# Kernel tuning notes

Hardware: AMD Instinct MI355X
Metric: run time of the kernel (lower is better)

Reference implementation:

```python
import jax, jax.numpy as jnp
import numpy as np

# ---- config (matches init_kwargs) ----
B, C_IN, L, T = 32, 12, 1024, 64
C1, C2, K = 64, 128, 7
PAD = K // 2
NUM_CLASSES = 4
GAIN = 2.0
TH1, TH2 = 0.5, 0.5
TAU1, TAU2 = 1.0, 0.9
RESET = 0.0


def setup_inputs() -> dict:
    key = jax.random.key(0)
    ks = jax.random.split(key, 7)
    x = jax.random.normal(ks[0], (B, C_IN, L, T), dtype=jnp.float32)
    w1 = jax.random.normal(ks[1], (C1, C_IN, K), dtype=jnp.float32) * 0.1
    b1 = jax.random.normal(ks[2], (C1,), dtype=jnp.float32) * 0.01
    w2 = jax.random.normal(ks[3], (C2, C1, K), dtype=jnp.float32) * 0.05
    b2 = jax.random.normal(ks[4], (C2,), dtype=jnp.float32) * 0.01
    fc_w = jax.random.normal(ks[5], (NUM_CLASSES, C2), dtype=jnp.float32) * 0.1
    fc_b = jax.random.normal(ks[6], (NUM_CLASSES,), dtype=jnp.float32) * 0.01
    return {"x": x, "w1": w1, "b1": b1, "w2": w2, "b2": b2, "fc_w": fc_w, "fc_b": fc_b}


def _conv1d(x, w, b):
    # x: [B, Cin, L], w: [Cout, Cin, K] -> [B, Cout, L] (same padding)
    y = jax.lax.conv_general_dilated(
        x, w, window_strides=(1,), padding=[(PAD, PAD)],
        dimension_numbers=("NCW", "OIW", "NCW"))
    return y + b[None, :, None]


def _lif(v, inp, tau, thresh):
    # v <- v + (inp - v)/tau; spike = (v >= thresh); reset spiked neurons
    v = v + (inp - v) / tau
    spike = (v >= thresh).astype(inp.dtype)
    v = jnp.where(spike > 0, jnp.asarray(RESET, inp.dtype), v)
    return v, spike


def reference(x, w1, b1, w2, b2, fc_w, fc_b):
    # QuantStub/DeQuantStub are identity in the fp32 eager model.
    xs = jnp.transpose(x, (3, 0, 1, 2))  # [T, B, C_IN, L]

    def step(carry, xt):
        v1, v2, acc = carry
        h1 = _conv1d(xt, w1, b1) * GAIN
        v1, s1 = _lif(v1, h1, TAU1, TH1)
        h2 = _conv1d(s1, w2, b2) * GAIN
        v2, s2 = _lif(v2, h2, TAU2, TH2)
        return (v1, v2, acc + s2), None

    v1_0 = jnp.zeros((B, C1, L), x.dtype)
    v2_0 = jnp.zeros((B, C2, L), x.dtype)
    acc0 = jnp.zeros((B, C2, L), x.dtype)
    (_, _, acc), _ = jax.lax.scan(step, (v1_0, v2_0, acc0), xs)

    out = acc / jnp.asarray(T, x.dtype)          # [B, C2, L]
    out = jnp.mean(out, axis=-1)                  # AdaptiveAvgPool1d(1) + squeeze
    return out @ fc_w.T + fc_b                    # [B, NUM_CLASSES]
```

## Files before the change

### kernel.cpp

```cpp
#include <hip/hip_runtime.h>
#include <hip/hip_bf16.h>
#include <cstdint>

#define B_   32
#define CIN  12
#define L_   1024
#define T_   64
#define C1_  64
#define C2_  128
#define K_   7
#define PAD_ 3

typedef __attribute__((ext_vector_type(8))) short short8;
typedef __attribute__((ext_vector_type(4))) float float4v;

#define WS_S1T   0ull
#define WS_W2HI  268435456ull
#define WS_W1F   (WS_W2HI + 114688ull)
#define WS_ACCL  (WS_W1F + 32768ull)

static __device__ __forceinline__ ushort bf16_hi(float f) {
    __hip_bfloat16 h = __float2bfloat16(f);
    ushort u; __builtin_memcpy(&u, &h, 2); return u;
}
static __device__ __forceinline__ float bf16_back(ushort u) {
    __hip_bfloat16 h; __builtin_memcpy(&h, &u, 2); return __bfloat162float(h);
}

__global__ __launch_bounds__(256) void k0_prep_w2(const float* __restrict__ w2,
                                                  ushort* __restrict__ w2hi) {
    int i = blockIdx.x * 256 + threadIdx.x;
    if (i >= C2_ * K_ * C1_) return;
    int c2 = i / (K_ * C1_);
    int r_ = i % (K_ * C1_);
    int kk = r_ / C1_;
    int c1 = r_ % C1_;
    float w = w2[(c2 * C1_ + c1) * K_ + kk];
    ushort uh = bf16_hi(w);
    int h    = c1 >> 5;
    int c1r  = c1 & 31;
    int e    = c1r >> 4;
    int kq   = (c1r >> 2) & 3;
    int rr   = c1r & 3;
    int j    = e * 4 + rr;
    int mt   = c2 >> 4;
    int lane = kq * 16 + (c2 & 15);
    int o    = ((((kk * 2 + h) * 8 + mt) * 64) + lane) * 8 + j;
    w2hi[o] = uh;
}

__global__ __launch_bounds__(256) void k0_prep_w1(const float* __restrict__ w1,
                                                  ushort* __restrict__ w1f) {
    int i = blockIdx.x * 256 + threadIdx.x;
    if (i >= 16384) return;
    int j    = i & 7;
    int lane = (i >> 3) & 63;
    int mf   = (i >> 9) & 3;
    int ks   = (i >> 11) & 3;
    int cp   = i >> 13;
    int k    = ks * 32 + (lane >> 4) * 8 + j;
    int dl   = k >> 4;
    int slot = k & 15;
    int c1   = mf * 16 + (lane & 15);
    float v  = (slot < CIN && dl < K_) ? w1[(c1 * CIN + slot) * K_ + dl] : 0.0f;
    ushort hi = bf16_hi(v);
    float  rem = v - bf16_back(hi);
    ushort lo = bf16_hi(rem);
    w1f[i] = cp ? lo : hi;
}

__global__ __launch_bounds__(256, 2) void k1_conv1_mfma(const float* __restrict__ x,
                                                        const ushort* __restrict__ w1f,
                                                        const float* __restrict__ b1,
                                                        ushort* __restrict__ s1t) {
    __shared__ __align__(16) ushort S[10 * 2048];
    int tid  = threadIdx.x;
    int lane = tid & 63;
    int wl   = tid >> 6;
    int b    = blockIdx.y;
    int bx   = blockIdx.x;
    int swz  = ((bx & 7) << 5) | (bx >> 3);
    int lb   = swz * 4;

    #pragma unroll
    for (int it = 0; it < 5; ++it) {
        int u  = it * 256 + tid;
        int t  = u & 63;
        int h2 = (u >> 6) & 1;
        int lp = u >> 7;
        int gl = lb + lp - PAD_;
        bool ok = (gl >= 0) && (gl < L_);
        short8 hv, lv;
        #pragma unroll
        for (int jj = 0; jj < 8; ++jj) {
            int cin = h2 * 8 + jj;
            float v = (ok && cin < CIN)
                ? x[(((size_t)b * CIN + cin) * L_ + gl) * T_ + t] : 0.0f;
            ushort hb = bf16_hi(v);
            ushort lo = bf16_hi(v - bf16_back(hb));
            hv[jj] = (short)hb;
            lv[jj] = (short)lo;
        }
        int nt = t >> 4, t15 = t & 15;
        int base = lp * 2048 + nt * 256 + h2 * 128 + t15 * 8;
        *(short8*)&S[base]        = hv;
        *(short8*)&S[base + 1024] = lv;
    }
    __syncthreads();

    int t15 = lane & 15;
    int h2l = (lane >> 4) & 1;
    int kqh = lane >> 5;

    float4v acc[4][4];
    #pragma unroll
    for (int i = 0; i < 4; ++i)
        #pragma unroll
        for (int jn = 0; jn < 4; ++jn)
            acc[i][jn] = (float4v){0.0f, 0.0f, 0.0f, 0.0f};

    #pragma unroll
    for (int ks = 0; ks < 4; ++ks) {
        int dtap = ks * 2 + kqh;
        int lpr  = (dtap == 7) ? 0 : (wl + dtap);
        int rb   = lpr * 2048 + h2l * 128 + t15 * 8;
        short8 bh[4], bl[4];
        #pragma unroll
        for (int nt = 0; nt < 4; ++nt) {
            bh[nt] = *(const short8*)&S[rb + nt * 256];
            bl[nt] = *(const short8*)&S[rb + nt * 256 + 1024];
        }
        #pragma unroll
        for (int mf = 0; mf < 4; ++mf) {
            const ushort* ap = w1f + ((size_t)(ks * 4 + mf) * 64 + lane) * 8;
            short8 ah = *(const short8*)ap;
            short8 al = *(const short8*)(ap + 8192);
            #pragma unroll
            for (int nt = 0; nt < 4; ++nt) {
                acc[mf][nt] = __builtin_amdgcn_mfma_f32_16x16x32_bf16(ah, bh[nt], acc[mf][nt], 0, 0, 0);
                acc[mf][nt] = __builtin_amdgcn_mfma_f32_16x16x32_bf16(al, bh[nt], acc[mf][nt], 0, 0, 0);
                acc[mf][nt] = __builtin_amdgcn_mfma_f32_16x16x32_bf16(ah, bl[nt], acc[mf][nt], 0, 0, 0);
            }
        }
    }

    int l  = lb + wl;
    int kq = lane >> 4;
    #pragma unroll
    for (int h = 0; h < 2; ++h) {
        float4v be0 = *(const float4v*)&b1[h * 32 + kq * 4];
        float4v be1 = *(const float4v*)&b1[h * 32 + 16 + kq * 4];
        #pragma unroll
        for (int nt = 0; nt < 4; ++nt) {
            uint s0 = (acc[2 * h][nt][0] + be0[0] >= 0.25f) ? 0x3F80u : 0u;
            uint s1 = (acc[2 * h][nt][1] + be0[1] >= 0.25f) ? 0x3F80u : 0u;
            uint s2 = (acc[2 * h][nt][2] + be0[2] >= 0.25f) ? 0x3F80u : 0u;
            uint s3 = (acc[2 * h][nt][3] + be0[3] >= 0.25f) ? 0x3F80u : 0u;
            uint s4 = (acc[2 * h + 1][nt][0] + be1[0] >= 0.25f) ? 0x3F80u : 0u;
            uint s5 = (acc[2 * h + 1][nt][1] + be1[1] >= 0.25f) ? 0x3F80u : 0u;
            uint s6 = (acc[2 * h + 1][nt][2] + be1[2] >= 0.25f) ? 0x3F80u : 0u;
            uint s7 = (acc[2 * h + 1][nt][3] + be1[3] >= 0.25f) ? 0x3F80u : 0u;
            uint4 u4 = { s0 | (s1 << 16), s2 | (s3 << 16),
                         s4 | (s5 << 16), s6 | (s7 << 16) };
            size_t off = ((((size_t)b * L_ + l) * 2 + h) * T_ + (nt * 16 + t15)) * 32 + kq * 8;
            *(uint4*)&s1t[off] = u4;
        }
    }
}

__global__ __launch_bounds__(256, 2) void k2_conv2_lif(const ushort* __restrict__ s1t,
                                                       const ushort* __restrict__ w2hi,
                                                       const float* __restrict__ b2,
                                                       float* __restrict__ accl) {
    __shared__ __align__(16) unsigned char lds_raw[33792];
    ushort* S = (ushort*)lds_raw;
    int tid    = threadIdx.x;
    int wv     = tid >> 6;
    int lane   = tid & 63;
    int wm     = wv >> 1;
    int wn     = wv & 1;
    int b      = blockIdx.y;
    int lb     = blockIdx.x * 2;
    int lane15 = lane & 15;
    int kq     = lane >> 4;

    float4v acc[4][4];
    #pragma unroll
    for (int i = 0; i < 4; ++i)
        #pragma unroll
        for (int j = 0; j < 4; ++j)
            acc[i][j] = (float4v){0.0f, 0.0f, 0.0f, 0.0f};

    #pragma unroll 1
    for (int h = 0; h < 2; ++h) {
        __syncthreads();
        #pragma unroll
        for (int it = 0; it < 2; ++it) {
            int u  = it * 256 + tid;
            int lp = u >> 6, t = u & 63;
            int gl = lb + lp - PAD_;
            uint4 v0 = {0,0,0,0}, v1 = {0,0,0,0}, v2 = {0,0,0,0}, v3 = {0,0,0,0};
            if (gl >= 0 && gl < L_) {
                const uint4* q = (const uint4*)&s1t[((((size_t)b * L_ + gl) * 2 + h) * T_ + t) * 32];
                v0 = q[0]; v1 = q[1]; v2 = q[2]; v3 = q[3];
            }
            int nt = t >> 4, t15 = t & 15;
            *(uint4*)&S[(((lp * 4 + nt) * 4 + 0) * 16 + t15) * 8] = v0;
            *(uint4*)&S[(((lp * 4 + nt) * 4 + 1) * 16 + t15) * 8] = v1;
            *(uint4*)&S[(((lp * 4 + nt) * 4 + 2) * 16 + t15) * 8] = v2;
            *(uint4*)&S[(((lp * 4 + nt) * 4 + 3) * 16 + t15) * 8] = v3;
        }
        __syncthreads();
        #pragma unroll 2
        for (int kk = 0; kk < K_; ++kk) {
            int lp = wn + kk;
            short8 bf[4];
            #pragma unroll
            for (int nt = 0; nt < 4; ++nt)
                bf[nt] = *(const short8*)&S[(((lp * 4 + nt) * 4) * 16) * 8 + lane * 8];
            #pragma unroll
            for (int mf = 0; mf < 4; ++mf) {
                size_t aoff = ((((size_t)kk * 2 + h) * 8 + wm * 4 + mf) * 64 + lane) * 8;
                short8 ahi = *(const short8*)&w2hi[aoff];
                #pragma unroll
                for (int nt = 0; nt < 4; ++nt)
                    acc[mf][nt] = __builtin_amdgcn_mfma_f32_16x16x32_bf16(ahi, bf[nt], acc[mf][nt], 0, 0, 0);
            }
        }
    }
    __syncthreads();

    float* E = ((float*)lds_raw) + wv * (64 * 33);
    int l = lb + wn;
    const float Af = 1.0f - 1.0f / 0.9f;
    const float Cs = 2.0f / 0.9f;
    #pragma unroll
    for (int chunk = 0; chunk < 2; ++chunk) {
        #pragma unroll
        for (int mfl = 0; mfl < 2; ++mfl) {
            int mf = chunk * 2 + mfl;
            #pragma unroll
            for (int nt = 0; nt < 4; ++nt) {
                int t = nt * 16 + lane15;
                #pragma unroll
                for (int r = 0; r < 4; ++r)
                    E[t * 33 + mfl * 16 + kq * 4 + r] = acc[mf][nt][r];
            }
        }
        __builtin_amdgcn_s_waitcnt(0);
        if (lane < 32) {
            int c2 = wm * 64 + chunk * 32 + lane;
            float D = b2[c2] * Cs;
            float v = 0.0f;
            uint cnt = 0u;
            #pragma unroll 8
            for (int t = 0; t < T_; ++t) {
                float e = fmaf(E[t * 33 + lane], Cs, D);
                v = fmaf(Af, v, e);
                bool sp = (v >= 0.5f);
                cnt += sp ? 1u : 0u;
                v = sp ? 0.0f : v;
            }
            accl[((size_t)b * L_ + l) * C2_ + c2] = (float)cnt;
        }
        __builtin_amdgcn_s_waitcnt(0);
    }
}

__global__ __launch_bounds__(128) void k3_fc(const float* __restrict__ accl,
                                             const float* __restrict__ fcw,
                                             const float* __restrict__ fcb,
                                             float* __restrict__ out) {
    __shared__ float p[C2_];
    int b = blockIdx.x, c = threadIdx.x;
    float s = 0.0f;
    for (int l = 0; l < L_; ++l)
        s += accl[((size_t)b * L_ + l) * C2_ + c];
    p[c] = s * (1.0f / 65536.0f);
    __syncthreads();
    if (c < 4) {
        float o = fcb[c];
        #pragma unroll 8
        for (int i = 0; i < C2_; ++i)
            o = fmaf(fcw[c * C2_ + i], p[i], o);
        out[b * 4 + c] = o;
    }
}

extern "C" void kernel_launch(void* const* d_in, const int* in_sizes, int n_in,
                              void* d_out, int out_size, void* d_ws, size_t ws_size,
                              hipStream_t stream) {
    const float* x   = (const float*)d_in[0];
    const float* w1  = (const float*)d_in[1];
    const float* b1  = (const float*)d_in[2];
    const float* w2  = (const float*)d_in[3];
    const float* b2  = (const float*)d_in[4];
    const float* fcw = (const float*)d_in[5];
    const float* fcb = (const float*)d_in[6];
    float* out = (float*)d_out;

    char* ws = (char*)d_ws;
    ushort* s1t  = (ushort*)(ws + WS_S1T);
    ushort* w2h  = (ushort*)(ws + WS_W2HI);
    ushort* w1f  = (ushort*)(ws + WS_W1F);
    float*  accl = (float*)(ws + WS_ACCL);

    k0_prep_w2<<<dim3((C2_ * K_ * C1_ + 255) / 256), dim3(256), 0, stream>>>(w2, w2h);
    k0_prep_w1<<<dim3(64), dim3(256), 0, stream>>>(w1, w1f);
    k1_conv1_mfma<<<dim3(L_ / 4, B_), dim3(256), 0, stream>>>(x, w1f, b1, s1t);
    k2_conv2_lif<<<dim3(L_ / 2, B_), dim3(256), 0, stream>>>(s1t, w2h, b2, accl);
    k3_fc<<<dim3(B_), dim3(128), 0, stream>>>(accl, fcw, fcb, out);
}
```

Measured before the change: 572.2 us.

## Widen conv2 block to four positions, all channels per wave, atomic pooling

The conv2+LIF kernel now handles four sequence positions per block, with each wave covering all 128 output channels for one position. This raises reuse of the staged spike tile, since 10 positions of halo now serve 4 outputs instead of 5 serving 2. Block indices are swizzled across positions, the per-position spike counts are atomically added into a per-batch pooled buffer zeroed in the prep kernel, and the FC kernel shrinks to a single small block. The cost is more accumulator registers (8x4 MFMA tiles), a larger LDS footprint that may reduce occupancy, and float atomic contention on the pool buffer.

```diff
diff --git a/kernel.cpp b/kernel.cpp
--- a/kernel.cpp
+++ b/kernel.cpp
@@ -17,7 +17,7 @@
 #define WS_S1T   0ull
 #define WS_W2HI  268435456ull
 #define WS_W1F   (WS_W2HI + 114688ull)
-#define WS_ACCL  (WS_W1F + 32768ull)
+#define WS_POOL  (WS_W1F + 32768ull)
 
 static __device__ __forceinline__ ushort bf16_hi(float f) {
     __hip_bfloat16 h = __float2bfloat16(f);
@@ -28,8 +28,10 @@
 }
 
 __global__ __launch_bounds__(256) void k0_prep_w2(const float* __restrict__ w2,
-                                                  ushort* __restrict__ w2hi) {
+                                                  ushort* __restrict__ w2hi,
+                                                  float* __restrict__ pool) {
     int i = blockIdx.x * 256 + threadIdx.x;
+    if (i < B_ * C2_) pool[i] = 0.0f;
     if (i >= C2_ * K_ * C1_) return;
     int c2 = i / (K_ * C1_);
     int r_ = i % (K_ * C1_);
@@ -171,22 +173,22 @@
 __global__ __launch_bounds__(256, 2) void k2_conv2_lif(const ushort* __restrict__ s1t,
                                                        const ushort* __restrict__ w2hi,
                                                        const float* __restrict__ b2,
-                                                       float* __restrict__ accl) {
-    __shared__ __align__(16) unsigned char lds_raw[33792];
+                                                       float* __restrict__ pool) {
+    __shared__ __align__(16) unsigned char lds_raw[69632];
     ushort* S = (ushort*)lds_raw;
     int tid    = threadIdx.x;
     int wv     = tid >> 6;
     int lane   = tid & 63;
-    int wm     = wv >> 1;
-    int wn     = wv & 1;
     int b      = blockIdx.y;
-    int lb     = blockIdx.x * 2;
+    int bx     = blockIdx.x;
+    int swz    = ((bx & 7) << 5) | (bx >> 3);
+    int lb     = swz * 4;
     int lane15 = lane & 15;
     int kq     = lane >> 4;
 
-    float4v acc[4][4];
-    #pragma unroll
-    for (int i = 0; i < 4; ++i)
+    float4v acc[8][4];
+    #pragma unroll
+    for (int i = 0; i < 8; ++i)
         #pragma unroll
         for (int j = 0; j < 4; ++j)
             acc[i][j] = (float4v){0.0f, 0.0f, 0.0f, 0.0f};
@@ -195,32 +197,35 @@
     for (int h = 0; h < 2; ++h) {
         __syncthreads();
         #pragma unroll
-        for (int it = 0; it < 2; ++it) {
-            int u  = it * 256 + tid;
-            int lp = u >> 6, t = u & 63;
-            int gl = lb + lp - PAD_;
-            uint4 v0 = {0,0,0,0}, v1 = {0,0,0,0}, v2 = {0,0,0,0}, v3 = {0,0,0,0};
-            if (gl >= 0 && gl < L_) {
-                const uint4* q = (const uint4*)&s1t[((((size_t)b * L_ + gl) * 2 + h) * T_ + t) * 32];
-                v0 = q[0]; v1 = q[1]; v2 = q[2]; v3 = q[3];
+        for (int it = 0; it < 3; ++it) {
+            int u = it * 256 + tid;
+            if (u < 640) {
+                int lp = u >> 6, t = u & 63;
+                int gl = lb + lp - PAD_;
+                uint4 v0 = {0,0,0,0}, v1 = {0,0,0,0}, v2 = {0,0,0,0}, v3 = {0,0,0,0};
+                if (gl >= 0 && gl < L_) {
+                    const uint4* q = (const uint4*)&s1t[((((size_t)b * L_ + gl) * 2 + h) * T_ + t) * 32];
+                    v0 = q[0]; v1 = q[1]; v2 = q[2]; v3 = q[3];
+                }
+                int nt = t >> 4, t15 = t & 15;
+                int base = lp * 2048 + nt * 512 + t15 * 8;
+                *(uint4*)&S[base]       = v0;
+                *(uint4*)&S[base + 128] = v1;
+                *(uint4*)&S[base + 256] = v2;
+                *(uint4*)&S[base + 384] = v3;
             }
-            int nt = t >> 4, t15 = t & 15;
-            *(uint4*)&S[(((lp * 4 + nt) * 4 + 0) * 16 + t15) * 8] = v0;
-            *(uint4*)&S[(((lp * 4 + nt) * 4 + 1) * 16 + t15) * 8] = v1;
-            *(uint4*)&S[(((lp * 4 + nt) * 4 + 2) * 16 + t15) * 8] = v2;
-            *(uint4*)&S[(((lp * 4 + nt) * 4 + 3) * 16 + t15) * 8] = v3;
         }
         __syncthreads();
         #pragma unroll 2
         for (int kk = 0; kk < K_; ++kk) {
-            int lp = wn + kk;
+            int lp = wv + kk;
             short8 bf[4];
             #pragma unroll
             for (int nt = 0; nt < 4; ++nt)
-                bf[nt] = *(const short8*)&S[(((lp * 4 + nt) * 4) * 16) * 8 + lane * 8];
+                bf[nt] = *(const short8*)&S[lp * 2048 + nt * 512 + lane * 8];
             #pragma unroll
-            for (int mf = 0; mf < 4; ++mf) {
-                size_t aoff = ((((size_t)kk * 2 + h) * 8 + wm * 4 + mf) * 64 + lane) * 8;
+            for (int mf = 0; mf < 8; ++mf) {
+                int aoff = (((kk * 2 + h) * 8 + mf) * 64 + lane) * 8;
                 short8 ahi = *(const short8*)&w2hi[aoff];
                 #pragma unroll
                 for (int nt = 0; nt < 4; ++nt)
@@ -230,61 +235,48 @@
     }
     __syncthreads();
 
-    float* E = ((float*)lds_raw) + wv * (64 * 33);
-    int l = lb + wn;
+    float* E = ((float*)lds_raw) + wv * (64 * 68);
     const float Af = 1.0f - 1.0f / 0.9f;
     const float Cs = 2.0f / 0.9f;
     #pragma unroll
     for (int chunk = 0; chunk < 2; ++chunk) {
         #pragma unroll
-        for (int mfl = 0; mfl < 2; ++mfl) {
-            int mf = chunk * 2 + mfl;
+        for (int mfl = 0; mfl < 4; ++mfl) {
             #pragma unroll
-            for (int nt = 0; nt < 4; ++nt) {
-                int t = nt * 16 + lane15;
-                #pragma unroll
-                for (int r = 0; r < 4; ++r)
-                    E[t * 33 + mfl * 16 + kq * 4 + r] = acc[mf][nt][r];
-            }
+            for (int nt = 0; nt < 4; ++nt)
+                *(float4v*)&E[(nt * 16 + lane15) * 68 + mfl * 16 + kq * 4] = acc[chunk * 4 + mfl][nt];
         }
         __builtin_amdgcn_s_waitcnt(0);
-        if (lane < 32) {
-            int c2 = wm * 64 + chunk * 32 + lane;
+        {
+            int c2 = chunk * 64 + lane;
             float D = b2[c2] * Cs;
             float v = 0.0f;
             uint cnt = 0u;
             #pragma unroll 8
             for (int t = 0; t < T_; ++t) {
-                float e = fmaf(E[t * 33 + lane], Cs, D);
+                float e = fmaf(E[t * 68 + lane], Cs, D);
                 v = fmaf(Af, v, e);
                 bool sp = (v >= 0.5f);
                 cnt += sp ? 1u : 0u;
                 v = sp ? 0.0f : v;
             }
-            accl[((size_t)b * L_ + l) * C2_ + c2] = (float)cnt;
+            atomicAdd(&pool[b * C2_ + c2], (float)cnt);
         }
         __builtin_amdgcn_s_waitcnt(0);
     }
 }
 
-__global__ __launch_bounds__(128) void k3_fc(const float* __restrict__ accl,
+__global__ __launch_bounds__(128) void k3_fc(const float* __restrict__ pool,
                                              const float* __restrict__ fcw,
                                              const float* __restrict__ fcb,
                                              float* __restrict__ out) {
-    __shared__ float p[C2_];
-    int b = blockIdx.x, c = threadIdx.x;
-    float s = 0.0f;
-    for (int l = 0; l < L_; ++l)
-        s += accl[((size_t)b * L_ + l) * C2_ + c];
-    p[c] = s * (1.0f / 65536.0f);
-    __syncthreads();
-    if (c < 4) {
-        float o = fcb[c];
-        #pragma unroll 8
-        for (int i = 0; i < C2_; ++i)
-            o = fmaf(fcw[c * C2_ + i], p[i], o);
-        out[b * 4 + c] = o;
-    }
+    int i = threadIdx.x;
+    int b = i >> 2, c = i & 3;
+    float o = fcb[c];
+    #pragma unroll 8
+    for (int c2 = 0; c2 < C2_; ++c2)
+        o = fmaf(fcw[c * C2_ + c2], pool[b * C2_ + c2] * (1.0f / 65536.0f), o);
+    out[b * 4 + c] = o;
 }
 
 extern "C" void kernel_launch(void* const* d_in, const int* in_sizes, int n_in,
@@ -303,11 +295,11 @@
     ushort* s1t  = (ushort*)(ws + WS_S1T);
     ushort* w2h  = (ushort*)(ws + WS_W2HI);
     ushort* w1f  = (ushort*)(ws + WS_W1F);
-    float*  accl = (float*)(ws + WS_ACCL);
-
-    k0_prep_w2<<<dim3((C2_ * K_ * C1_ + 255) / 256), dim3(256), 0, stream>>>(w2, w2h);
+    float*  pool = (float*)(ws + WS_POOL);
+
+    k0_prep_w2<<<dim3((C2_ * K_ * C1_ + 255) / 256), dim3(256), 0, stream>>>(w2, w2h, pool);
     k0_prep_w1<<<dim3(64), dim3(256), 0, stream>>>(w1, w1f);
     k1_conv1_mfma<<<dim3(L_ / 4, B_), dim3(256), 0, stream>>>(x, w1f, b1, s1t);
-    k2_conv2_lif<<<dim3(L_ / 2, B_), dim3(256), 0, stream>>>(s1t, w2h, b2, accl);
-    k3_fc<<<dim3(B_), dim3(128), 0, stream>>>(accl, fcw, fcb, out);
-}
+    k2_conv2_lif<<<dim3(L_ / 4, B_), dim3(256), 0, stream>>>(s1t, w2h, b2, pool);
+    k3_fc<<<dim3(1), dim3(128), 0, stream>>>(pool, fcw, fcb, out);
+}
```

Result: slower. 609.4 us (+6.5%).
